# Performance work log

Hardware: AMD Instinct MI355X
Metric: run time of the kernel (lower is better)

## Reference

```python
import jax, jax.numpy as jnp
import numpy as np

EMBED_DIM = 1024
N_HEADS = 16
HEAD_DIM = EMBED_DIM // N_HEADS
SCALE = 1.0 / np.sqrt(HEAD_DIM)


def setup_inputs() -> dict:
    key = jax.random.key(0)
    ks = jax.random.split(key, 11)
    B, S, D = 4, 2048, EMBED_DIM
    lim = 1.0 / np.sqrt(D)
    def lin(kk):
        kw, kb = jax.random.split(kk)
        W = jax.random.uniform(kw, (D, D), jnp.float32, -lim, lim)
        b = jax.random.uniform(kb, (D,), jnp.float32, -lim, lim)
        return W, b
    Wq, bq = lin(ks[0])
    Wk, bk = lin(ks[1])
    Wv, bv = lin(ks[2])
    Wo, bo = lin(ks[3])
    q = jax.random.normal(ks[4], (B, S, D), jnp.float32)
    k = jax.random.normal(ks[5], (B, S, D), jnp.float32)
    v = jax.random.normal(ks[6], (B, S, D), jnp.float32)
    return {"q": q, "k": k, "v": v,
            "Wq": Wq, "bq": bq, "Wk": Wk, "bk": bk,
            "Wv": Wv, "bv": bv, "Wo": Wo, "bo": bo}


def reference(q, k, v, Wq, bq, Wk, bk, Wv, bv, Wo, bo):
    B, Sq, D = q.shape
    Sk = k.shape[1]
    # linear projections (torch Linear: x @ W.T + b)
    qh = (q @ Wq.T + bq).reshape(B, Sq, N_HEADS, HEAD_DIM).transpose(0, 2, 1, 3)
    kh = (k @ Wk.T + bk).reshape(B, Sk, N_HEADS, HEAD_DIM).transpose(0, 2, 1, 3)
    vh = (v @ Wv.T + bv).reshape(B, Sk, N_HEADS, HEAD_DIM).transpose(0, 2, 1, 3)
    # scaled dot-product attention, no mask, dropout_p=0
    scores = jnp.einsum('bhqd,bhkd->bhqk', qh, kh) * SCALE  # [B,H,Sq,Sk]
    weights = jax.nn.softmax(scores, axis=-1)
    ctx = jnp.einsum('bhqk,bhkd->bhqd', weights, vh)
    ctx = ctx.transpose(0, 2, 1, 3).reshape(B, Sq, D)
    return ctx @ Wo.T + bo
```

## Files before the change

### kernel.cpp

```cpp
#include <hip/hip_runtime.h>
#include <hip/hip_bf16.h>
#include <stdint.h>

#define B_SZ 4
#define SEQ  2048
#define DM   1024
#define NH   16
#define HD   64
#define MTOT (B_SZ*SEQ)
#define QS_LOG2E 0.18033688011112042f
#define M0SHIFT  24.0f

typedef __attribute__((ext_vector_type(8))) short bf16x8;
typedef __attribute__((ext_vector_type(4))) float f32x4;

#if __has_builtin(__builtin_amdgcn_exp2f)
__device__ __forceinline__ float fexp2(float x) { return __builtin_amdgcn_exp2f(x); }
#else
__device__ __forceinline__ float fexp2(float x) {
  float r; asm("v_exp_f32 %0, %1" : "=v"(r) : "v"(x)); return r;
}
#endif

__device__ __forceinline__ unsigned short f2b(float f) {
  union { float f; unsigned int i; } v; v.f = f;
  unsigned int r = v.i + 0x7fffu + ((v.i >> 16) & 1u);
  return (unsigned short)(r >> 16);
}

#define GPTR __attribute__((address_space(1)))
#define LPTR __attribute__((address_space(3)))
__device__ __forceinline__ void gl_lds16(const void* g, void* l) {
  __builtin_amdgcn_global_load_lds((GPTR const unsigned int*)g,
                                   (LPTR unsigned int*)l, 16, 0, 0);
}

__global__ __launch_bounds__(256) void conv3(const float* __restrict__ a,
                                             const float* __restrict__ b,
                                             const float* __restrict__ c,
                                             unsigned short* __restrict__ oa,
                                             unsigned short* __restrict__ ob,
                                             unsigned short* __restrict__ oc,
                                             int n) {
  const float* in = (blockIdx.z == 0) ? a : (blockIdx.z == 1) ? b : c;
  unsigned short* out = (blockIdx.z == 0) ? oa : (blockIdx.z == 1) ? ob : oc;
  int i = (blockIdx.x * 256 + threadIdx.x) * 8;
  int stride = gridDim.x * 256 * 8;
  for (; i < n; i += stride) {
    float4 x = *(const float4*)(in + i);
    float4 y = *(const float4*)(in + i + 4);
    ushort4 u0; u0.x = f2b(x.x); u0.y = f2b(x.y); u0.z = f2b(x.z); u0.w = f2b(x.w);
    ushort4 u1; u1.x = f2b(y.x); u1.y = f2b(y.y); u1.z = f2b(y.z); u1.w = f2b(y.w);
    *(ushort4*)(out + i)     = u0;
    *(ushort4*)(out + i + 4) = u1;
  }
}
__global__ __launch_bounds__(256) void conv4(const float* __restrict__ a,
                                             const float* __restrict__ b,
                                             const float* __restrict__ c,
                                             const float* __restrict__ d,
                                             unsigned short* __restrict__ oa,
                                             unsigned short* __restrict__ ob,
                                             unsigned short* __restrict__ oc,
                                             unsigned short* __restrict__ od,
                                             int n) {
  const float* in = (blockIdx.z == 0) ? a : (blockIdx.z == 1) ? b
                  : (blockIdx.z == 2) ? c : d;
  unsigned short* out = (blockIdx.z == 0) ? oa : (blockIdx.z == 1) ? ob
                      : (blockIdx.z == 2) ? oc : od;
  int i = (blockIdx.x * 256 + threadIdx.x) * 8;
  int stride = gridDim.x * 256 * 8;
  for (; i < n; i += stride) {
    float4 x = *(const float4*)(in + i);
    float4 y = *(const float4*)(in + i + 4);
    ushort4 u0; u0.x = f2b(x.x); u0.y = f2b(x.y); u0.z = f2b(x.z); u0.w = f2b(x.w);
    ushort4 u1; u1.x = f2b(y.x); u1.y = f2b(y.y); u1.z = f2b(y.z); u1.w = f2b(y.w);
    *(ushort4*)(out + i)     = u0;
    *(ushort4*)(out + i + 4) = u1;
  }
}

__device__ __forceinline__ void stage_glds(const unsigned short* __restrict__ src,
                                           int ld, char* lds, int t) {
  const int gbase = t & ~63;
  const int lane  = t & 63;
  #pragma unroll
  for (int i = 0; i < 4; ++i) {
    int gb  = i*256 + gbase;
    int g   = gb + lane;
    int row = g >> 3;
    int cg  = (g & 7) ^ (row & 7);
    gl_lds16(src + (size_t)row*ld + cg*8, lds + (size_t)gb*16);
  }
}
__device__ __forceinline__ void stage_f32(const float* __restrict__ src, int ld,
                                          unsigned short* lds, int t) {
  #pragma unroll
  for (int i = 0; i < 8; ++i) {
    int e   = i*1024 + t*4;
    int row = e >> 6;
    int c4  = (e >> 2) & 15;
    float4 f = *(const float4*)(src + (size_t)row*ld + c4*4);
    ushort4 u;
    u.x = f2b(f.x); u.y = f2b(f.y); u.z = f2b(f.z); u.w = f2b(f.w);
    int hi = (row*64 + c4*4) ^ ((row & 7) << 3);
    *(ushort4*)&lds[hi] = u;
  }
}

template<int AF32, int BF32, int OUTF32>
__global__ __launch_bounds__(256, 2) void gemm_bias(
    const void* __restrict__ Xv,
    const void* __restrict__ Wv,
    const float* __restrict__ bias,
    void* __restrict__ Cout,
    int M, int N, int Kd, float oscale)
{
  __shared__ __align__(16) unsigned short As[128*64];
  __shared__ __align__(16) unsigned short Bs[128*64];
  const int t    = threadIdx.x;
  const int lane = t & 63;
  const int w    = t >> 6;
  const int wm   = w >> 1, wn = w & 1;
  const int m0   = blockIdx.y * 128;
  const int n0   = blockIdx.x * 128;

  f32x4 acc[4][4] = {};

  for (int k0 = 0; k0 < Kd; k0 += 64) {
    __syncthreads();
    if (AF32) stage_f32((const float*)Xv + (size_t)m0*Kd + k0, Kd, As, t);
    else      stage_glds((const unsigned short*)Xv + (size_t)m0*Kd + k0, Kd, (char*)As, t);
    if (BF32) stage_f32((const float*)Wv + (size_t)n0*Kd + k0, Kd, Bs, t);
    else      stage_glds((const unsigned short*)Wv + (size_t)n0*Kd + k0, Kd, (char*)Bs, t);
    __syncthreads();

    #pragma unroll
    for (int kk = 0; kk < 2; ++kk) {
      bf16x8 af[4], bfr[4];
      #pragma unroll
      for (int mt = 0; mt < 4; ++mt) {
        int r  = wm*64 + mt*16 + (lane & 15);
        int hi = (r*64 + kk*32 + (lane >> 4)*8) ^ ((r & 7) << 3);
        af[mt] = *(const bf16x8*)&As[hi];
      }
      #pragma unroll
      for (int nt = 0; nt < 4; ++nt) {
        int r  = wn*64 + nt*16 + (lane & 15);
        int hi = (r*64 + kk*32 + (lane >> 4)*8) ^ ((r & 7) << 3);
        bfr[nt] = *(const bf16x8*)&Bs[hi];
      }
      #pragma unroll
      for (int mt = 0; mt < 4; ++mt)
        #pragma unroll
        for (int nt = 0; nt < 4; ++nt)
          acc[mt][nt] = __builtin_amdgcn_mfma_f32_16x16x32_bf16(
              af[mt], bfr[nt], acc[mt][nt], 0, 0, 0);
    }
  }

  #pragma unroll
  for (int nt = 0; nt < 4; ++nt) {
    int col = n0 + wn*64 + nt*16 + (lane & 15);
    float bv = bias[col];
    #pragma unroll
    for (int mt = 0; mt < 4; ++mt) {
      #pragma unroll
      for (int j = 0; j < 4; ++j) {
        int rrow = m0 + wm*64 + mt*16 + (lane >> 4)*4 + j;
        float val = (acc[mt][nt][j] + bv) * oscale;
        if (OUTF32)
          ((float*)Cout)[(size_t)rrow*N + col] = val;
        else
          ((unsigned short*)Cout)[(size_t)rrow*N + col] = f2b(val);
      }
    }
  }
}

__global__ __launch_bounds__(256, 4) void attn_fwd(
    const unsigned short* __restrict__ Qb,
    const unsigned short* __restrict__ Kb,
    const unsigned short* __restrict__ Vb,
    unsigned short* __restrict__ Ob)
{
  __shared__ __align__(16) unsigned short Buf[4][64*64];

  const int t    = threadIdx.x;
  const int lane = t & 63;
  const int w    = t >> 6;
  const int l15  = lane & 15;
  const int quad = lane >> 4;
  const int bh   = blockIdx.y;
  const int b    = bh >> 4, h = bh & 15;
  const int q0   = blockIdx.x * 64;
  const int gbase = t & ~63;

  const size_t headoff = ((size_t)b*SEQ)*DM + (size_t)h*HD;
  const unsigned short* Qh = Qb + headoff;
  const unsigned short* Kh = Kb + headoff;
  const unsigned short* Vh = Vb + headoff;

  const int jp   = (t & 31) * 2;
  const int seg  = t >> 5;
  const int slot0 = ((jp >> 5) & 1)*32 + ((jp >> 2) & 3)*8 + ((jp >> 4) & 1)*4 + (jp & 3);
  const unsigned short* vsrc = Vh + (size_t)jp*DM + seg*8;

  const int krow = (gbase + lane) >> 3;
  (void)krow;

  #pragma unroll
  for (int i = 0; i < 2; ++i) {
    int gb  = i*256 + gbase;
    int g   = gb + lane;
    int row = g >> 3;
    int cg  = (g & 7) ^ (row & 7);
    gl_lds16(Qh + (size_t)(q0 + row)*DM + cg*8, (char*)Buf[3] + (size_t)gb*16);
    gl_lds16(Kh + (size_t)row*DM + cg*8,        (char*)Buf[2] + (size_t)gb*16);
  }
  bf16x8 pvA0 = *(const bf16x8*)(vsrc);
  bf16x8 pvA1 = *(const bf16x8*)(vsrc + DM);
  bf16x8 pvB0 = *(const bf16x8*)(vsrc + 64*DM);
  bf16x8 pvB1 = *(const bf16x8*)(vsrc + 65*DM);
  __syncthreads();

  bf16x8 qf[2];
  #pragma unroll
  for (int kk = 0; kk < 2; ++kk) {
    int r  = w*16 + l15;
    int hi = (r*64 + kk*32 + quad*8) ^ ((r & 7) << 3);
    qf[kk] = *(const bf16x8*)&Buf[3][hi];
  }
  #pragma unroll
  for (int e = 0; e < 8; ++e) {
    int d = seg*8 + e;
    unsigned int pk = (unsigned int)(unsigned short)pvA0[e]
                    | ((unsigned int)(unsigned short)pvA1[e] << 16);
    *(unsigned int*)&Buf[0][(d*64 + slot0) ^ ((d & 7) << 3)] = pk;
  }
  __syncthreads();

  #pragma unroll
  for (int i = 0; i < 2; ++i) {
    int gb  = i*256 + gbase;
    int g   = gb + lane;
    int row = g >> 3;
    int cg  = (g & 7) ^ (row & 7);
    gl_lds16(Kh + (size_t)(64 + row)*DM + cg*8, (char*)Buf[3] + (size_t)gb*16);
  }
  #pragma unroll
  for (int e = 0; e < 8; ++e) {
    int d = seg*8 + e;
    unsigned int pk = (unsigned int)(unsigned short)pvB0[e]
                    | ((unsigned int)(unsigned short)pvB1[e] << 16);
    *(unsigned int*)&Buf[1][(d*64 + slot0) ^ ((d & 7) << 3)] = pk;
  }

  float l_acc = 0.f;
  f32x4 oacc[4] = {};
  const f32x4 mseed = {-M0SHIFT, -M0SHIFT, -M0SHIFT, -M0SHIFT};

  auto tile = [&](const unsigned short* Kc, const unsigned short* Vc) {
    f32x4 sac[4] = {mseed, mseed, mseed, mseed};
    #pragma unroll
    for (int kk = 0; kk < 2; ++kk) {
      #pragma unroll
      for (int nt = 0; nt < 4; ++nt) {
        int r  = nt*16 + l15;
        int hi = (r*64 + kk*32 + quad*8) ^ ((r & 7) << 3);
        bf16x8 kf = *(const bf16x8*)&Kc[hi];
        sac[nt] = __builtin_amdgcn_mfma_f32_16x16x32_bf16(kf, qf[kk], sac[nt], 0, 0, 0);
      }
    }
    float p[4][4];
    float rs = 0.f;
    #pragma unroll
    for (int nt = 0; nt < 4; ++nt)
      #pragma unroll
      for (int j = 0; j < 4; ++j) {
        p[nt][j] = fexp2(sac[nt][j]);
        rs += p[nt][j];
      }
    l_acc += rs;

    union { bf16x8 v; unsigned int u[4]; } P0, P1;
    #pragma unroll
    for (int k2 = 0; k2 < 4; ++k2) {
      int nt = k2 >> 1, a = (k2 & 1)*2;
      asm("v_cvt_pk_bf16_f32 %0, %1, %2" : "=v"(P0.u[k2]) : "v"(p[nt][a]), "v"(p[nt][a+1]));
      asm("v_cvt_pk_bf16_f32 %0, %1, %2" : "=v"(P1.u[k2]) : "v"(p[2+nt][a]), "v"(p[2+nt][a+1]));
    }
    #pragma unroll
    for (int ks = 0; ks < 2; ++ks) {
      bf16x8 pf = ks ? P1.v : P0.v;
      #pragma unroll
      for (int dt = 0; dt < 4; ++dt) {
        int d  = dt*16 + l15;
        int hi = (d*64 + ks*32 + quad*8) ^ ((d & 7) << 3);
        bf16x8 vf = *(const bf16x8*)&Vc[hi];
        oacc[dt] = __builtin_amdgcn_mfma_f32_16x16x32_bf16(vf, pf, oacc[dt], 0, 0, 0);
      }
    }
  };

  auto stageK = [&](int kv0, unsigned short* dst) {
    #pragma unroll
    for (int i = 0; i < 2; ++i) {
      int gb  = i*256 + gbase;
      int g   = gb + lane;
      int row = g >> 3;
      int cg  = (g & 7) ^ (row & 7);
      gl_lds16(Kh + (size_t)(kv0 + row)*DM + cg*8, (char*)dst + (size_t)gb*16);
    }
  };
  auto writeV = [&](const bf16x8& v0, const bf16x8& v1, unsigned short* dst) {
    #pragma unroll
    for (int e = 0; e < 8; ++e) {
      int d = seg*8 + e;
      unsigned int pk = (unsigned int)(unsigned short)v0[e]
                      | ((unsigned int)(unsigned short)v1[e] << 16);
      *(unsigned int*)&dst[(d*64 + slot0) ^ ((d & 7) << 3)] = pk;
    }
  };

  for (int tk = 0; tk < SEQ/64; tk += 2) {
    const bool pa = (tk + 2 < SEQ/64);
    const bool pb = (tk + 3 < SEQ/64);
    if (pa) {
      const unsigned short* s = vsrc + (size_t)(tk + 2)*64*DM;
      pvA0 = *(const bf16x8*)(s);
      pvA1 = *(const bf16x8*)(s + DM);
    }
    tile(Buf[2], Buf[0]);
    __syncthreads();
    if (pa) { stageK((tk + 2)*64, Buf[2]); writeV(pvA0, pvA1, Buf[0]); }
    if (pb) {
      const unsigned short* s = vsrc + (size_t)(tk + 3)*64*DM;
      pvB0 = *(const bf16x8*)(s);
      pvB1 = *(const bf16x8*)(s + DM);
    }
    tile(Buf[3], Buf[1]);
    __syncthreads();
    if (pb) { stageK((tk + 3)*64, Buf[3]); writeV(pvB0, pvB1, Buf[1]); }
  }

  {
    float l = l_acc;
    l += __shfl_xor(l, 16);
    l += __shfl_xor(l, 32);
    float rl = 1.0f / l;
    int qrow = q0 + w*16 + l15;
    #pragma unroll
    for (int dt = 0; dt < 4; ++dt) {
      ushort4 u;
      u.x = f2b(oacc[dt][0]*rl);
      u.y = f2b(oacc[dt][1]*rl);
      u.z = f2b(oacc[dt][2]*rl);
      u.w = f2b(oacc[dt][3]*rl);
      *(ushort4*)&Ob[headoff + (size_t)qrow*DM + dt*16 + quad*4] = u;
    }
  }
}

extern "C" void kernel_launch(void* const* d_in, const int* in_sizes, int n_in,
                              void* d_out, int out_size, void* d_ws, size_t ws_size,
                              hipStream_t stream) {
  const float* q  = (const float*)d_in[0];
  const float* k  = (const float*)d_in[1];
  const float* v  = (const float*)d_in[2];
  const float* Wq = (const float*)d_in[3];
  const float* bq = (const float*)d_in[4];
  const float* Wk = (const float*)d_in[5];
  const float* bk = (const float*)d_in[6];
  const float* Wv = (const float*)d_in[7];
  const float* bv = (const float*)d_in[8];
  const float* Wo = (const float*)d_in[9];
  const float* bo = (const float*)d_in[10];

  const size_t MD  = (size_t)MTOT * DM;
  const size_t WSZ = (size_t)DM * DM;
  unsigned short* ws = (unsigned short*)d_ws;

  dim3 blk(256);
  dim3 gproj(DM/128, MTOT/128);
  dim3 gattn(SEQ/64, B_SZ*NH);

  const size_t need_big = (6*MD + 4*WSZ) * 2;
  const size_t need_mid = (4*MD + 1*WSZ) * 2;

  if (ws_size >= need_big) {
    unsigned short* qB  = ws;
    unsigned short* kB  = ws + MD;
    unsigned short* vB  = ws + 2*MD;
    unsigned short* Qp  = ws + 3*MD;
    unsigned short* Kp  = ws + 4*MD;
    unsigned short* Vp  = ws + 5*MD;
    unsigned short* WqB = ws + 6*MD;
    unsigned short* WkB = WqB + WSZ;
    unsigned short* WvB = WqB + 2*WSZ;
    unsigned short* WoB = WqB + 3*WSZ;
    unsigned short* Cp  = qB;

    hipLaunchKernelGGL(conv3, dim3(1024,1,3), blk, 0, stream, q, k, v, qB, kB, vB, (int)MD);
    hipLaunchKernelGGL(conv4, dim3(512,1,4),  blk, 0, stream, Wq, Wk, Wv, Wo, WqB, WkB, WvB, WoB, (int)WSZ);

    hipLaunchKernelGGL((gemm_bias<0,0,0>), gproj, blk, 0, stream, (const void*)qB, (const void*)WqB, bq, (void*)Qp, MTOT, DM, DM, QS_LOG2E);
    hipLaunchKernelGGL((gemm_bias<0,0,0>), gproj, blk, 0, stream, (const void*)kB, (const void*)WkB, bk, (void*)Kp, MTOT, DM, DM, 1.0f);
    hipLaunchKernelGGL((gemm_bias<0,0,0>), gproj, blk, 0, stream, (const void*)vB, (const void*)WvB, bv, (void*)Vp, MTOT, DM, DM, 1.0f);
    hipLaunchKernelGGL(attn_fwd, gattn, blk, 0, stream, Qp, Kp, Vp, Cp);
    hipLaunchKernelGGL((gemm_bias<0,0,1>), gproj, blk, 0, stream, (const void*)Cp, (const void*)WoB, bo, d_out, MTOT, DM, DM, 1.0f);
  } else if (ws_size >= need_mid) {
    unsigned short* Qp  = ws;
    unsigned short* Kp  = ws + MD;
    unsigned short* Vp  = ws + 2*MD;
    unsigned short* Cp  = ws + 3*MD;
    unsigned short* WqB = Cp;
    unsigned short* WkB = Cp + WSZ;
    unsigned short* WvB = Cp + 2*WSZ;
    unsigned short* WoB = ws + 4*MD;

    hipLaunchKernelGGL(conv4, dim3(512,1,4), blk, 0, stream, Wq, Wk, Wv, Wo, WqB, WkB, WvB, WoB, (int)WSZ);

    hipLaunchKernelGGL((gemm_bias<1,0,0>), gproj, blk, 0, stream, (const void*)q, (const void*)WqB, bq, (void*)Qp, MTOT, DM, DM, QS_LOG2E);
    hipLaunchKernelGGL((gemm_bias<1,0,0>), gproj, blk, 0, stream, (const void*)k, (const void*)WkB, bk, (void*)Kp, MTOT, DM, DM, 1.0f);
    hipLaunchKernelGGL((gemm_bias<1,0,0>), gproj, blk, 0, stream, (const void*)v, (const void*)WvB, bv, (void*)Vp, MTOT, DM, DM, 1.0f);
    hipLaunchKernelGGL(attn_fwd, gattn, blk, 0, stream, Qp, Kp, Vp, Cp);
    hipLaunchKernelGGL((gemm_bias<0,0,1>), gproj, blk, 0, stream, (const void*)Cp, (const void*)WoB, bo, d_out, MTOT, DM, DM, 1.0f);
  } else {
    unsigned short* Qp = ws;
    unsigned short* Kp = ws + MD;
    unsigned short* Vp = ws + 2*MD;
    unsigned short* Cp = ws + 3*MD;

    hipLaunchKernelGGL((gemm_bias<1,1,0>), gproj, blk, 0, stream, (const void*)q, (const void*)Wq, bq, (void*)Qp, MTOT, DM, DM, QS_LOG2E);
    hipLaunchKernelGGL((gemm_bias<1,1,0>), gproj, blk, 0, stream, (const void*)k, (const void*)Wk, bk, (void*)Kp, MTOT, DM, DM, 1.0f);
    hipLaunchKernelGGL((gemm_bias<1,1,0>), gproj, blk, 0, stream, (const void*)v, (const void*)Wv, bv, (void*)Vp, MTOT, DM, DM, 1.0f);
    hipLaunchKernelGGL(attn_fwd, gattn, blk, 0, stream, Qp, Kp, Vp, Cp);
    hipLaunchKernelGGL((gemm_bias<0,1,1>), gproj, blk, 0, stream, (const void*)Cp, (const void*)Wo, bo, d_out, MTOT, DM, DM, 1.0f);
  }
}
```

Before: 254.2 us.

## Process 128 query rows per attention block so K/V tiles are reused twice

Each attention workgroup now handles 128 query rows instead of 64, with each wave computing two 16-row query fragments against every staged K/V tile. This halves the K/V global loads and LDS staging per query and doubles the MFMA work per LDS fragment read. It also wraps the MFMA phases in s_setprio to favour matrix issue. The costs are higher register pressure, which may hurt occupancy under launch_bounds(256,4), and half as many workgroups in the grid.

After: 471.6 us. 85.5% more time.

```diff
diff --git a/kernel.cpp b/kernel.cpp
--- a/kernel.cpp
+++ b/kernel.cpp
@@ -193,7 +193,7 @@
   const int quad = lane >> 4;
   const int bh   = blockIdx.y;
   const int b    = bh >> 4, h = bh & 15;
-  const int q0   = blockIdx.x * 64;
+  const int q0   = blockIdx.x * 128;
   const int gbase = t & ~63;
 
   const size_t headoff = ((size_t)b*SEQ)*DM + (size_t)h*HD;
@@ -206,17 +206,16 @@
   const int slot0 = ((jp >> 5) & 1)*32 + ((jp >> 2) & 3)*8 + ((jp >> 4) & 1)*4 + (jp & 3);
   const unsigned short* vsrc = Vh + (size_t)jp*DM + seg*8;
 
-  const int krow = (gbase + lane) >> 3;
-  (void)krow;
-
-  #pragma unroll
-  for (int i = 0; i < 2; ++i) {
-    int gb  = i*256 + gbase;
-    int g   = gb + lane;
-    int row = g >> 3;
-    int cg  = (g & 7) ^ (row & 7);
-    gl_lds16(Qh + (size_t)(q0 + row)*DM + cg*8, (char*)Buf[3] + (size_t)gb*16);
-    gl_lds16(Kh + (size_t)row*DM + cg*8,        (char*)Buf[2] + (size_t)gb*16);
+  {
+    unsigned short* Qlds = &Buf[2][0];
+    #pragma unroll
+    for (int i = 0; i < 4; ++i) {
+      int gb  = i*256 + gbase;
+      int g   = gb + lane;
+      int row = g >> 3;
+      int cg  = (g & 7) ^ (row & 7);
+      gl_lds16(Qh + (size_t)(q0 + row)*DM + cg*8, (char*)Qlds + (size_t)gb*16);
+    }
   }
   bf16x8 pvA0 = *(const bf16x8*)(vsrc);
   bf16x8 pvA1 = *(const bf16x8*)(vsrc + DM);
@@ -224,84 +223,29 @@
   bf16x8 pvB1 = *(const bf16x8*)(vsrc + 65*DM);
   __syncthreads();
 
-  bf16x8 qf[2];
-  #pragma unroll
-  for (int kk = 0; kk < 2; ++kk) {
-    int r  = w*16 + l15;
-    int hi = (r*64 + kk*32 + quad*8) ^ ((r & 7) << 3);
-    qf[kk] = *(const bf16x8*)&Buf[3][hi];
-  }
-  #pragma unroll
-  for (int e = 0; e < 8; ++e) {
-    int d = seg*8 + e;
-    unsigned int pk = (unsigned int)(unsigned short)pvA0[e]
-                    | ((unsigned int)(unsigned short)pvA1[e] << 16);
-    *(unsigned int*)&Buf[0][(d*64 + slot0) ^ ((d & 7) << 3)] = pk;
-  }
+  bf16x8 qfA[2], qfB[2];
+  {
+    const unsigned short* Qlds = &Buf[2][0];
+    #pragma unroll
+    for (int kk = 0; kk < 2; ++kk) {
+      int rA  = w*32 + l15;
+      int rB  = w*32 + 16 + l15;
+      qfA[kk] = *(const bf16x8*)&Qlds[(rA*64 + kk*32 + quad*8) ^ ((rA & 7) << 3)];
+      qfB[kk] = *(const bf16x8*)&Qlds[(rB*64 + kk*32 + quad*8) ^ ((rB & 7) << 3)];
+    }
+  }
+  auto writeV = [&](const bf16x8& v0, const bf16x8& v1, unsigned short* dst) {
+    #pragma unroll
+    for (int e = 0; e < 8; ++e) {
+      int d = seg*8 + e;
+      unsigned int pk = (unsigned int)(unsigned short)v0[e]
+                      | ((unsigned int)(unsigned short)v1[e] << 16);
+      *(unsigned int*)&dst[(d*64 + slot0) ^ ((d & 7) << 3)] = pk;
+    }
+  };
+  writeV(pvA0, pvA1, Buf[0]);
+  writeV(pvB0, pvB1, Buf[1]);
   __syncthreads();
-
-  #pragma unroll
-  for (int i = 0; i < 2; ++i) {
-    int gb  = i*256 + gbase;
-    int g   = gb + lane;
-    int row = g >> 3;
-    int cg  = (g & 7) ^ (row & 7);
-    gl_lds16(Kh + (size_t)(64 + row)*DM + cg*8, (char*)Buf[3] + (size_t)gb*16);
-  }
-  #pragma unroll
-  for (int e = 0; e < 8; ++e) {
-    int d = seg*8 + e;
-    unsigned int pk = (unsigned int)(unsigned short)pvB0[e]
-                    | ((unsigned int)(unsigned short)pvB1[e] << 16);
-    *(unsigned int*)&Buf[1][(d*64 + slot0) ^ ((d & 7) << 3)] = pk;
-  }
-
-  float l_acc = 0.f;
-  f32x4 oacc[4] = {};
-  const f32x4 mseed = {-M0SHIFT, -M0SHIFT, -M0SHIFT, -M0SHIFT};
-
-  auto tile = [&](const unsigned short* Kc, const unsigned short* Vc) {
-    f32x4 sac[4] = {mseed, mseed, mseed, mseed};
-    #pragma unroll
-    for (int kk = 0; kk < 2; ++kk) {
-      #pragma unroll
-      for (int nt = 0; nt < 4; ++nt) {
-        int r  = nt*16 + l15;
-        int hi = (r*64 + kk*32 + quad*8) ^ ((r & 7) << 3);
-        bf16x8 kf = *(const bf16x8*)&Kc[hi];
-        sac[nt] = __builtin_amdgcn_mfma_f32_16x16x32_bf16(kf, qf[kk], sac[nt], 0, 0, 0);
-      }
-    }
-    float p[4][4];
-    float rs = 0.f;
-    #pragma unroll
-    for (int nt = 0; nt < 4; ++nt)
-      #pragma unroll
-      for (int j = 0; j < 4; ++j) {
-        p[nt][j] = fexp2(sac[nt][j]);
-        rs += p[nt][j];
-      }
-    l_acc += rs;
-
-    union { bf16x8 v; unsigned int u[4]; } P0, P1;
-    #pragma unroll
-    for (int k2 = 0; k2 < 4; ++k2) {
-      int nt = k2 >> 1, a = (k2 & 1)*2;
-      asm("v_cvt_pk_bf16_f32 %0, %1, %2" : "=v"(P0.u[k2]) : "v"(p[nt][a]), "v"(p[nt][a+1]));
-      asm("v_cvt_pk_bf16_f32 %0, %1, %2" : "=v"(P1.u[k2]) : "v"(p[2+nt][a]), "v"(p[2+nt][a+1]));
-    }
-    #pragma unroll
-    for (int ks = 0; ks < 2; ++ks) {
-      bf16x8 pf = ks ? P1.v : P0.v;
-      #pragma unroll
-      for (int dt = 0; dt < 4; ++dt) {
-        int d  = dt*16 + l15;
-        int hi = (d*64 + ks*32 + quad*8) ^ ((d & 7) << 3);
-        bf16x8 vf = *(const bf16x8*)&Vc[hi];
-        oacc[dt] = __builtin_amdgcn_mfma_f32_16x16x32_bf16(vf, pf, oacc[dt], 0, 0, 0);
-      }
-    }
-  };
 
   auto stageK = [&](int kv0, unsigned short* dst) {
     #pragma unroll
@@ -313,14 +257,76 @@
       gl_lds16(Kh + (size_t)(kv0 + row)*DM + cg*8, (char*)dst + (size_t)gb*16);
     }
   };
-  auto writeV = [&](const bf16x8& v0, const bf16x8& v1, unsigned short* dst) {
-    #pragma unroll
-    for (int e = 0; e < 8; ++e) {
-      int d = seg*8 + e;
-      unsigned int pk = (unsigned int)(unsigned short)v0[e]
-                      | ((unsigned int)(unsigned short)v1[e] << 16);
-      *(unsigned int*)&dst[(d*64 + slot0) ^ ((d & 7) << 3)] = pk;
-    }
+  stageK(0,  Buf[2]);
+  stageK(64, Buf[3]);
+  __syncthreads();
+
+  float lA = 0.f, lB = 0.f;
+  f32x4 oA[4] = {}, oB[4] = {};
+  const f32x4 mseed = {-M0SHIFT, -M0SHIFT, -M0SHIFT, -M0SHIFT};
+
+  auto tile = [&](const unsigned short* Kc, const unsigned short* Vc) {
+    f32x4 sA[4] = {mseed, mseed, mseed, mseed};
+    f32x4 sB[4] = {mseed, mseed, mseed, mseed};
+    __builtin_amdgcn_s_setprio(1);
+    #pragma unroll
+    for (int kk = 0; kk < 2; ++kk) {
+      #pragma unroll
+      for (int nt = 0; nt < 4; ++nt) {
+        int r  = nt*16 + l15;
+        int hi = (r*64 + kk*32 + quad*8) ^ ((r & 7) << 3);
+        bf16x8 kf = *(const bf16x8*)&Kc[hi];
+        sA[nt] = __builtin_amdgcn_mfma_f32_16x16x32_bf16(kf, qfA[kk], sA[nt], 0, 0, 0);
+        sB[nt] = __builtin_amdgcn_mfma_f32_16x16x32_bf16(kf, qfB[kk], sB[nt], 0, 0, 0);
+      }
+    }
+    __builtin_amdgcn_s_setprio(0);
+
+    union { bf16x8 v; unsigned int u[4]; } PA0, PA1, PB0, PB1;
+    {
+      float p[4][4]; float rs = 0.f;
+      #pragma unroll
+      for (int nt = 0; nt < 4; ++nt)
+        #pragma unroll
+        for (int j = 0; j < 4; ++j) { p[nt][j] = fexp2(sA[nt][j]); rs += p[nt][j]; }
+      lA += rs;
+      #pragma unroll
+      for (int k2 = 0; k2 < 4; ++k2) {
+        int nt = k2 >> 1, a = (k2 & 1)*2;
+        asm("v_cvt_pk_bf16_f32 %0, %1, %2" : "=v"(PA0.u[k2]) : "v"(p[nt][a]), "v"(p[nt][a+1]));
+        asm("v_cvt_pk_bf16_f32 %0, %1, %2" : "=v"(PA1.u[k2]) : "v"(p[2+nt][a]), "v"(p[2+nt][a+1]));
+      }
+    }
+    {
+      float p[4][4]; float rs = 0.f;
+      #pragma unroll
+      for (int nt = 0; nt < 4; ++nt)
+        #pragma unroll
+        for (int j = 0; j < 4; ++j) { p[nt][j] = fexp2(sB[nt][j]); rs += p[nt][j]; }
+      lB += rs;
+      #pragma unroll
+      for (int k2 = 0; k2 < 4; ++k2) {
+        int nt = k2 >> 1, a = (k2 & 1)*2;
+        asm("v_cvt_pk_bf16_f32 %0, %1, %2" : "=v"(PB0.u[k2]) : "v"(p[nt][a]), "v"(p[nt][a+1]));
+        asm("v_cvt_pk_bf16_f32 %0, %1, %2" : "=v"(PB1.u[k2]) : "v"(p[2+nt][a]), "v"(p[2+nt][a+1]));
+      }
+    }
+
+    __builtin_amdgcn_s_setprio(1);
+    #pragma unroll
+    for (int ks = 0; ks < 2; ++ks) {
+      bf16x8 pfA = ks ? PA1.v : PA0.v;
+      bf16x8 pfB = ks ? PB1.v : PB0.v;
+      #pragma unroll
+      for (int dt = 0; dt < 4; ++dt) {
+        int d  = dt*16 + l15;
+        int hi = (d*64 + ks*32 + quad*8) ^ ((d & 7) << 3);
+        bf16x8 vf = *(const bf16x8*)&Vc[hi];
+        oA[dt] = __builtin_amdgcn_mfma_f32_16x16x32_bf16(vf, pfA, oA[dt], 0, 0, 0);
+        oB[dt] = __builtin_amdgcn_mfma_f32_16x16x32_bf16(vf, pfB, oB[dt], 0, 0, 0);
+      }
+    }
+    __builtin_amdgcn_s_setprio(0);
   };
 
   for (int tk = 0; tk < SEQ/64; tk += 2) {
@@ -345,19 +351,22 @@
   }
 
   {
-    float l = l_acc;
-    l += __shfl_xor(l, 16);
-    l += __shfl_xor(l, 32);
-    float rl = 1.0f / l;
-    int qrow = q0 + w*16 + l15;
+    float la = lA, lb = lB;
+    la += __shfl_xor(la, 16); la += __shfl_xor(la, 32);
+    lb += __shfl_xor(lb, 16); lb += __shfl_xor(lb, 32);
+    float rla = 1.0f / la, rlb = 1.0f / lb;
+    int qrowA = q0 + w*32 + l15;
+    int qrowB = qrowA + 16;
     #pragma unroll
     for (int dt = 0; dt < 4; ++dt) {
       ushort4 u;
-      u.x = f2b(oacc[dt][0]*rl);
-      u.y = f2b(oacc[dt][1]*rl);
-      u.z = f2b(oacc[dt][2]*rl);
-      u.w = f2b(oacc[dt][3]*rl);
-      *(ushort4*)&Ob[headoff + (size_t)qrow*DM + dt*16 + quad*4] = u;
+      u.x = f2b(oA[dt][0]*rla); u.y = f2b(oA[dt][1]*rla);
+      u.z = f2b(oA[dt][2]*rla); u.w = f2b(oA[dt][3]*rla);
+      *(ushort4*)&Ob[headoff + (size_t)qrowA*DM + dt*16 + quad*4] = u;
+      ushort4 v;
+      v.x = f2b(oB[dt][0]*rlb); v.y = f2b(oB[dt][1]*rlb);
+      v.z = f2b(oB[dt][2]*rlb); v.w = f2b(oB[dt][3]*rlb);
+      *(ushort4*)&Ob[headoff + (size_t)qrowB*DM + dt*16 + quad*4] = v;
     }
   }
 }
@@ -383,7 +392,7 @@
 
   dim3 blk(256);
   dim3 gproj(DM/128, MTOT/128);
-  dim3 gattn(SEQ/64, B_SZ*NH);
+  dim3 gattn(SEQ/128, B_SZ*NH);
 
   const size_t need_big = (6*MD + 4*WSZ) * 2;
   const size_t need_mid = (4*MD + 1*WSZ) * 2;
```
